# Performance work log

Measured on AMD Instinct MI355X. Metric: run time of the kernel, lower is better.

The kernel has to match this reference:

```python
import jax, jax.numpy as jnp
import numpy as np

LN_EPS = 1e-5
ALPHA_Q = 1.0

def _ln(t, g, b):
    mu = jnp.mean(t, -1, keepdims=True)
    var = jnp.var(t, -1, keepdims=True)
    return (t - mu) / jnp.sqrt(var + LN_EPS) * g + b

def _mlp(t, w1, b1, w2, b2):
    h = jax.nn.gelu(t @ w1.T + b1, approximate=False)
    return h @ w2.T + b2

def setup_inputs() -> dict:
    key = jax.random.key(0)
    B, N, L, E, H, D = 2, 2048, 2048, 1024, 16, 4
    ks = jax.random.split(key, 40)
    rn = lambda i, shape, sc: jax.random.normal(ks[i], shape, jnp.float32) * sc
    inp = {}
    inp['x'] = rn(0, (B, N, E), 1.0)
    inp['xp'] = jax.random.uniform(ks[1], (B, N, D), jnp.float32)
    inp['y'] = rn(2, (B, L, E), 1.0)
    inp['yp'] = jax.random.uniform(ks[3], (B, L, D), jnp.float32)
    inp['attn_mask'] = jax.random.uniform(ks[4], (1, 1, N, L), jnp.float32)
    # PositionEncoder params (torch Linear convention: weight [out,in])
    inp['p_w1'] = rn(5, (E, D), 1.0 / D)
    inp['p_b1'] = jax.random.uniform(ks[6], (E,), jnp.float32, 0.0, np.pi)
    inp['p_w2'] = rn(7, (E, D), 1.0 / D)
    inp['p_b2'] = jax.random.uniform(ks[8], (E,), jnp.float32, 0.0, np.pi)
    # QueryEncoder: LayerNorm + mlp1 + mlp2 (mlp0 is dead code in the source)
    inp['q_ln_g'] = jnp.ones((E,), jnp.float32); inp['q_ln_b'] = jnp.zeros((E,), jnp.float32)
    inp['q_m1_w1'] = rn(9, (2 * E, E), 0.02); inp['q_m1_b1'] = jnp.zeros((2 * E,), jnp.float32)
    inp['q_m1_w2'] = rn(10, (E, 2 * E), 0.02); inp['q_m1_b2'] = jnp.zeros((E,), jnp.float32)
    inp['q_m2_w1'] = rn(11, (2 * E, E), 0.02); inp['q_m2_b1'] = jnp.zeros((2 * E,), jnp.float32)
    inp['q_m2_w2'] = rn(12, (E, 2 * E), 0.02); inp['q_m2_b2'] = jnp.zeros((E,), jnp.float32)
    # KeyEncoder: LayerNorm + mlp1 (mlp0 dead code)
    inp['k_ln_g'] = jnp.ones((E,), jnp.float32); inp['k_ln_b'] = jnp.zeros((E,), jnp.float32)
    inp['k_m1_w1'] = rn(13, (2 * E, E), 0.02); inp['k_m1_b1'] = jnp.zeros((2 * E,), jnp.float32)
    inp['k_m1_w2'] = rn(14, (E, 2 * E), 0.02); inp['k_m1_b2'] = jnp.zeros((E,), jnp.float32)
    # V: LayerNorm + Linear
    inp['v_ln_g'] = jnp.ones((E,), jnp.float32); inp['v_ln_b'] = jnp.zeros((E,), jnp.float32)
    inp['v_w'] = rn(15, (E, E), 0.02); inp['v_b'] = jnp.zeros((E,), jnp.float32)
    # output projections
    inp['proj1_w'] = rn(16, (E, E), 0.02); inp['proj1_b'] = jnp.zeros((E,), jnp.float32)
    inp['proj2_w'] = rn(17, (E, D * H), 0.02); inp['proj2_b'] = jnp.zeros((E,), jnp.float32)
    return inp

def reference(x, xp, y, yp, attn_mask, p_w1, p_b1, p_w2, p_b2,
              q_ln_g, q_ln_b, q_m1_w1, q_m1_b1, q_m1_w2, q_m1_b2,
              q_m2_w1, q_m2_b1, q_m2_w2, q_m2_b2,
              k_ln_g, k_ln_b, k_m1_w1, k_m1_b1, k_m1_w2, k_m1_b2,
              v_ln_g, v_ln_b, v_w, v_b, proj1_w, proj1_b, proj2_w, proj2_b):
    B, N, E = x.shape
    L = y.shape[1]
    D = xp.shape[2]
    H = proj2_w.shape[1] // D
    C = E // H
    # PositionEncoder: query side with bias, key side without bias
    pxt = ALPHA_Q * xp
    xp1 = pxt @ p_w1.T + p_b1            # [B,N,E]
    xp2 = pxt @ p_w2.T + p_b2
    pyt = ALPHA_Q * yp
    yp1 = pyt @ p_w1.T                   # [B,L,E], no bias
    yp2 = pyt @ p_w2.T
    rh = lambda t: t.reshape(t.shape[0], -1, H, C)
    # QueryEncoder
    xn = _ln(x, q_ln_g, q_ln_b)
    x1 = _mlp(xn, q_m1_w1, q_m1_b1, q_m1_w2, q_m1_b2)
    x2 = _mlp(xn, q_m2_w1, q_m2_b1, q_m2_w2, q_m2_b2)
    q = jnp.concatenate([rh(x1 * jnp.cos(xp1)), rh(x1 * jnp.sin(xp1)),
                         rh(x2 * jnp.cos(xp2)), rh(x2 * jnp.sin(xp2))], axis=-1)  # [B,N,H,4C]
    # KeyEncoder (note: second cos/sin block is the raw position code)
    yn = _ln(y, k_ln_g, k_ln_b)
    y1 = _mlp(yn, k_m1_w1, k_m1_b1, k_m1_w2, k_m1_b2)
    k = jnp.concatenate([rh(y1 * jnp.cos(yp1)), rh(y1 * jnp.sin(yp1)),
                         rh(jnp.cos(yp2)), rh(jnp.sin(yp2))], axis=-1)            # [B,L,H,4C]
    scale = (4 * C) ** (-0.5)
    attn = jax.nn.softmax(jnp.einsum('bnhd,blhd->bhnl', q, k) * scale, axis=-1)
    # masked renormalization (mask applied AFTER softmax)
    eps = min(1e-8, 1.0 / L)
    attn = attn * attn_mask
    attn = attn / (jnp.sum(attn, axis=-1, keepdims=True) + eps)
    # values
    v = (_ln(y, v_ln_g, v_ln_b) @ v_w.T + v_b).reshape(B, L, H, C)
    out1 = jnp.einsum('bhnl,blhc->bnhc', attn, v).reshape(B, N, E) @ proj1_w.T + proj1_b
    out2 = jnp.einsum('bhnl,bld->bnhd', attn, yp) - xp[:, :, None, :]             # [B,N,H,D]
    out2 = out2.reshape(B, N, H * D) @ proj2_w.T + proj2_b
    return (out1 + out2, attn, xp)
```

## Files before the change

### kernel.cpp

```cpp
#include <hip/hip_runtime.h>
#include <math.h>
#include <stdint.h>

#define DEV static __device__ __forceinline__

typedef __bf16 bf16x8 __attribute__((ext_vector_type(8)));
typedef __bf16 bf16x4v __attribute__((ext_vector_type(4)));
typedef float f32x4 __attribute__((ext_vector_type(4)));

constexpr int Nn = 2048, Ll = 2048, Ee = 1024, Hh = 16;
constexpr float SCALE = 0.0625f;

constexpr size_t OFF_XN   = 0;
constexpr size_t OFF_YNK  = 8388608;
constexpr size_t OFF_YNV  = 16777216;
constexpr size_t OFF_H12  = 25165824;
constexpr size_t OFF_H3   = 58720256;
constexpr size_t OFF_X1   = 75497472;
constexpr size_t OFF_X2   = 83886080;
constexpr size_t OFF_Y1   = 92274688;
constexpr size_t OFF_QWS  = 100663296;
constexpr size_t OFF_KWS  = 134217728;
constexpr size_t OFF_VWS  = 167772160;
constexpr size_t OFF_DNV  = 176160768;
constexpr size_t OFF_YPT  = 176422912;
constexpr size_t OFF_MSK  = 176685056;
constexpr size_t OFF_AVZ  = 185073664;
constexpr size_t OFF_W1122= 193986560;
constexpr size_t OFF_W12  = 202375168;
constexpr size_t OFF_W22  = 206569472;
constexpr size_t OFF_WK1  = 210763776;
constexpr size_t OFF_WK2  = 214958080;
constexpr size_t OFF_WV   = 219152384;
constexpr size_t OFF_WP   = 221249536;
constexpr size_t OFF_EM   = 223477760;

DEV void gl2l(const void* g, void* l) {
  __builtin_amdgcn_global_load_lds((const __attribute__((address_space(1))) void*)g,
                                   (__attribute__((address_space(3))) void*)l, 16, 0, 0);
}

DEV float gelu_f(float v) {
  float x = v * 0.70710678118654752f;
  float ax = fabsf(x);
  float t = 1.f / fmaf(0.3275911f, ax, 1.f);
  float y = t * fmaf(t, fmaf(t, fmaf(t, fmaf(t, 1.061405429f, -1.453152027f),
                                     1.421413741f), -0.284496736f), 0.254829592f);
  float er = 1.f - y * __expf(-x * x);
  er = (x < 0.f) ? -er : er;
  return 0.5f * v * (1.f + er);
}

__launch_bounds__(256)
__global__ void prep_all(const float* __restrict__ s0, const float* __restrict__ s1,
                         const float* __restrict__ s2, const float* __restrict__ s3,
                         const float* __restrict__ s4, const float* __restrict__ s5,
                         const float* __restrict__ s6,
                         __bf16* __restrict__ d0, __bf16* __restrict__ d1,
                         __bf16* __restrict__ d2, __bf16* __restrict__ d3,
                         __bf16* __restrict__ d4, __bf16* __restrict__ d5,
                         __bf16* __restrict__ d6,
                         const float* __restrict__ pw1, const float* __restrict__ pw2,
                         __bf16* __restrict__ wp,
                         const float* __restrict__ mask, __bf16* __restrict__ mb,
                         const float* __restrict__ yp, __bf16* __restrict__ ypT) {
  int u = blockIdx.x * 256 + threadIdx.x;
  if (u < 3407872) {
    int seg = u >> 19, r = u & 524287;
    const float* s; __bf16* d;
    if      (seg == 0) { s = s0; d = d0; }
    else if (seg == 1) { s = s1; d = d1; }
    else if (seg == 2) { s = s2; d = d2; }
    else if (seg == 3) { s = s3; d = d3; }
    else if (seg == 4) { s = s4; d = d4; }
    else if (seg == 5) { s = s5; d = d5; }
    else               { s = s6; d = d6; }
    float4 v = ((const float4*)s)[r];
    bf16x4v o; o[0]=(__bf16)v.x; o[1]=(__bf16)v.y; o[2]=(__bf16)v.z; o[3]=(__bf16)v.w;
    ((bf16x4v*)d)[r] = o;
  } else if (u < 3686400) {
    int p = u - 3407872;
    int row = p / 272, c4 = p - row * 272;
    float4 v = (c4 < 256) ? ((const float4*)pw1)[row * 256 + c4]
                          : ((const float4*)pw2)[row * 16 + (c4 - 256)];
    bf16x4v o; o[0]=(__bf16)v.x; o[1]=(__bf16)v.y; o[2]=(__bf16)v.z; o[3]=(__bf16)v.w;
    *(bf16x4v*)(wp + (size_t)row * 1088 + (c4 << 2)) = o;
  } else if (u < 4734976) {
    int q = u - 3686400;
    float4 v = ((const float4*)mask)[q];
    bf16x4v o; o[0]=(__bf16)v.x; o[1]=(__bf16)v.y; o[2]=(__bf16)v.z; o[3]=(__bf16)v.w;
    ((bf16x4v*)mb)[q] = o;
  } else {
    int t0 = (u - 4734976) << 2;
    #pragma unroll
    for (int k = 0; k < 4; k++) {
      int i = t0 + k;
      int b = i >> 13, d = (i >> 11) & 3, l = i & 2047;
      ypT[i] = (__bf16)yp[(((size_t)b << 11) + l) * 4 + d];
    }
  }
}

__launch_bounds__(256)
__global__ void ln_all(const float* __restrict__ x, const float* __restrict__ y,
                       const float* __restrict__ qg, const float* __restrict__ qb,
                       const float* __restrict__ kg, const float* __restrict__ kb,
                       const float* __restrict__ vg, const float* __restrict__ vb,
                       __bf16* __restrict__ xn, __bf16* __restrict__ ynk,
                       __bf16* __restrict__ ynv) {
  const int t = blockIdx.x, tid = threadIdx.x;
  const bool isx = t < 4096;
  const int row = isx ? t : t - 4096;
  const float* src = (isx ? x : y) + (size_t)row * Ee;
  const float4 v = ((const float4*)src)[tid];
  float s = v.x + v.y + v.z + v.w;
  float q = v.x*v.x + v.y*v.y + v.z*v.z + v.w*v.w;
  #pragma unroll
  for (int o = 32; o > 0; o >>= 1) { s += __shfl_down(s, o); q += __shfl_down(q, o); }
  __shared__ float ls[4], lq[4];
  if ((tid & 63) == 0) { ls[tid >> 6] = s; lq[tid >> 6] = q; }
  __syncthreads();
  s = ls[0] + ls[1] + ls[2] + ls[3];
  q = lq[0] + lq[1] + lq[2] + lq[3];
  const float mu = s * (1.f / Ee);
  const float rstd = rsqrtf(q * (1.f / Ee) - mu * mu + 1e-5f);
  const int e0 = tid << 2;
  float h0 = (v.x - mu) * rstd, h1 = (v.y - mu) * rstd,
        h2 = (v.z - mu) * rstd, h3 = (v.w - mu) * rstd;
  if (isx) {
    bf16x4v o;
    o[0] = (__bf16)(h0 * qg[e0]   + qb[e0]);
    o[1] = (__bf16)(h1 * qg[e0+1] + qb[e0+1]);
    o[2] = (__bf16)(h2 * qg[e0+2] + qb[e0+2]);
    o[3] = (__bf16)(h3 * qg[e0+3] + qb[e0+3]);
    *(bf16x4v*)(xn + (size_t)row * Ee + e0) = o;
  } else {
    bf16x4v ok, ov;
    ok[0] = (__bf16)(h0 * kg[e0]   + kb[e0]);
    ok[1] = (__bf16)(h1 * kg[e0+1] + kb[e0+1]);
    ok[2] = (__bf16)(h2 * kg[e0+2] + kb[e0+2]);
    ok[3] = (__bf16)(h3 * kg[e0+3] + kb[e0+3]);
    ov[0] = (__bf16)(h0 * vg[e0]   + vb[e0]);
    ov[1] = (__bf16)(h1 * vg[e0+1] + vb[e0+1]);
    ov[2] = (__bf16)(h2 * vg[e0+2] + vb[e0+2]);
    ov[3] = (__bf16)(h3 * vg[e0+3] + vb[e0+3]);
    *(bf16x4v*)(ynk + (size_t)row * Ee + e0) = ok;
    *(bf16x4v*)(ynv + (size_t)row * Ee + e0) = ov;
  }
}

#define GEMM_CORE_BK64(BM_, A_, lda_, W_, ldw_, K_)                                   \
  const int w = tid >> 6, lane = tid & 63, g = lane >> 4, li = lane & 15;             \
  const int wm = (w >> 2) * (BM_ / 2), wn = (w & 3) << 6;                             \
  constexpr int MI = BM_ / 32;                                                        \
  f32x4 acc[MI][4];                                                                   \
  _Pragma("unroll")                                                                   \
  for (int i = 0; i < MI; i++)                                                        \
    _Pragma("unroll")                                                                 \
    for (int j = 0; j < 4; j++) acc[i][j] = (f32x4)0.f;                               \
  auto stage = [&](int buf, int kt) {                                                 \
    const int col0 = kt << 6;                                                         \
    _Pragma("unroll")                                                                 \
    for (int jj = 0; jj < BM_ / 64; jj++) {                                           \
      int c = (jj << 9) + tid;                                                        \
      int row = c >> 3, sl = c & 7;                                                   \
      int col = col0 + ((sl ^ (row & 7)) << 3);                                       \
      gl2l(A_ + (size_t)(m0 + row) * lda_ + col, (buf ? As1 : As0) + ((c - lane) << 3)); \
    }                                                                                 \
    _Pragma("unroll")                                                                 \
    for (int jj = 0; jj < 4; jj++) {                                                  \
      int c = (jj << 9) + tid;                                                        \
      int row = c >> 3, sl = c & 7;                                                   \
      int col = col0 + ((sl ^ (row & 7)) << 3);                                       \
      gl2l(W_ + (size_t)(n0 + row) * ldw_ + col, (buf ? Bs1 : Bs0) + ((c - lane) << 3)); \
    }                                                                                 \
  };                                                                                  \
  const int NT = (K_) >> 6;                                                           \
  stage(0, 0);                                                                        \
  for (int kt = 0; kt < NT; kt++) {                                                   \
    const int cur = kt & 1;                                                           \
    if (kt + 1 < NT) {                                                                \
      stage(cur ^ 1, kt + 1);                                                         \
      asm volatile("s_waitcnt vmcnt(%0)" :: "i"(BM_ / 64 + 4) : "memory");            \
    } else {                                                                          \
      asm volatile("s_waitcnt vmcnt(0)" ::: "memory");                                \
    }                                                                                 \
    __builtin_amdgcn_s_barrier();                                                     \
    __builtin_amdgcn_sched_barrier(0);                                                \
    const __bf16* Acur = cur ? As1 : As0;                                             \
    const __bf16* Bcur = cur ? Bs1 : Bs0;                                             \
    _Pragma("unroll")                                                                 \
    for (int ks = 0; ks < 2; ks++) {                                                  \
      bf16x8 af[MI], bw[4];                                                           \
      _Pragma("unroll")                                                               \
      for (int i = 0; i < MI; i++) {                                                  \
        int ra = wm + (i << 4) + li;                                                  \
        af[i] = *(const bf16x8*)(Acur + ra * 64 + ((((ks << 2) | g) ^ (ra & 7)) << 3)); \
      }                                                                               \
      _Pragma("unroll")                                                               \
      for (int j = 0; j < 4; j++) {                                                   \
        int rb = wn + (j << 4) + li;                                                  \
        bw[j] = *(const bf16x8*)(Bcur + rb * 64 + ((((ks << 2) | g) ^ (rb & 7)) << 3)); \
      }                                                                               \
      _Pragma("unroll")                                                               \
      for (int i = 0; i < MI; i++)                                                    \
        _Pragma("unroll")                                                             \
        for (int j = 0; j < 4; j++)                                                   \
          acc[i][j] = __builtin_amdgcn_mfma_f32_16x16x32_bf16(af[i], bw[j], acc[i][j], 0, 0, 0); \
    }                                                                                 \
    asm volatile("s_waitcnt lgkmcnt(0)" ::: "memory");                                \
    __builtin_amdgcn_sched_barrier(0);                                                \
    __builtin_amdgcn_s_barrier();                                                     \
  }

__launch_bounds__(512, 2)
__global__ void gemm_mlp1(const __bf16* __restrict__ xn, const __bf16* __restrict__ ynk,
                          const __bf16* __restrict__ w1122, const __bf16* __restrict__ wk1,
                          const float* __restrict__ qb1, const float* __restrict__ qb2,
                          const float* __restrict__ kb1,
                          __bf16* __restrict__ h12, __bf16* __restrict__ h3) {
  __shared__ __align__(16) __bf16 As0[256 * 64];
  __shared__ __align__(16) __bf16 As1[256 * 64];
  __shared__ __align__(16) __bf16 Bs0[256 * 64];
  __shared__ __align__(16) __bf16 Bs1[256 * 64];
  const int tid = threadIdx.x, bid = blockIdx.x;
  if (bid < 256) {
    const int m0 = (bid >> 4) << 8, n0 = (bid & 15) << 8;
    GEMM_CORE_BK64(256, xn, 1024, w1122, 1024, 1024)
    #pragma unroll
    for (int j = 0; j < 4; j++) {
      int n = n0 + wn + (j << 4) + li;
      float bias = (n < 2048) ? qb1[n] : qb2[n - 2048];
      #pragma unroll
      for (int i = 0; i < MI; i++) {
        #pragma unroll
        for (int r = 0; r < 4; r++) {
          int m = m0 + wm + (i << 4) + (g << 2) + r;
          h12[(size_t)m * 4096 + n] = (__bf16)gelu_f(acc[i][j][r] + bias);
        }
      }
    }
  } else {
    const int rr = bid - 256;
    const int m0 = (rr >> 3) << 7, n0 = (rr & 7) << 8;
    GEMM_CORE_BK64(128, ynk, 1024, wk1, 1024, 1024)
    #pragma unroll
    for (int j = 0; j < 4; j++) {
      int n = n0 + wn + (j << 4) + li;
      float bias = kb1[n];
      #pragma unroll
      for (int i = 0; i < MI; i++) {
        #pragma unroll
        for (int r = 0; r < 4; r++) {
          int m = m0 + wm + (i << 4) + (g << 2) + r;
          h3[(size_t)m * 2048 + n] = (__bf16)gelu_f(acc[i][j][r] + bias);
        }
      }
    }
  }
}

__launch_bounds__(512, 2)
__global__ void gemm_mlp2(const __bf16* __restrict__ h12, const __bf16* __restrict__ h3,
                          const __bf16* __restrict__ ynv,
                          const __bf16* __restrict__ w12, const __bf16* __restrict__ w22,
                          const __bf16* __restrict__ wk2, const __bf16* __restrict__ wv,
                          const float* __restrict__ bx1, const float* __restrict__ bx2,
                          const float* __restrict__ by1, const float* __restrict__ bv,
                          __bf16* __restrict__ x1, __bf16* __restrict__ x2,
                          __bf16* __restrict__ y1, __bf16* __restrict__ vT) {
  __shared__ __align__(16) __bf16 As0[256 * 64];
  __shared__ __align__(16) __bf16 As1[256 * 64];
  __shared__ __align__(16) __bf16 Bs0[256 * 64];
  __shared__ __align__(16) __bf16 Bs1[256 * 64];
  const int tid = threadIdx.x, bid = blockIdx.x;
  const int seg = bid >> 6, rr = bid & 63;
  const int m0 = (rr >> 2) << 8, n0 = (rr & 3) << 8;
  const __bf16* A; const __bf16* W; const float* bias; __bf16* out; int lda, K;
  if      (seg == 0) { A = h12;        lda = 4096; W = w12; bias = bx1; out = x1; K = 2048; }
  else if (seg == 1) { A = h12 + 2048; lda = 4096; W = w22; bias = bx2; out = x2; K = 2048; }
  else if (seg == 2) { A = h3;         lda = 2048; W = wk2; bias = by1; out = y1; K = 2048; }
  else               { A = ynv;        lda = 1024; W = wv;  bias = bv;  out = vT; K = 1024; }
  GEMM_CORE_BK64(256, A, lda, W, K, K)
  #pragma unroll
  for (int j = 0; j < 4; j++) {
    int n = n0 + wn + (j << 4) + li;
    float bs = bias[n];
    #pragma unroll
    for (int i = 0; i < MI; i++) {
      #pragma unroll
      for (int r = 0; r < 4; r++) {
        int m = m0 + wm + (i << 4) + (g << 2) + r;
        float v = acc[i][j][r] + bs;
        if (seg == 3) {
          int bb = m >> 11, l = m & 2047, hh = n >> 6, cc = n & 63;
          vT[(((size_t)(bb * Hh + hh) * 64 + cc) << 11) + l] = (__bf16)v;
        } else {
          out[(size_t)m * 1024 + n] = (__bf16)v;
        }
      }
    }
  }
}

__launch_bounds__(256)
__global__ void build_qk(const __bf16* __restrict__ x1, const __bf16* __restrict__ x2,
                         const float* __restrict__ xp,
                         const __bf16* __restrict__ y1, const float* __restrict__ yp,
                         const float* __restrict__ pw1, const float* __restrict__ pb1,
                         const float* __restrict__ pw2, const float* __restrict__ pb2,
                         __bf16* __restrict__ q_ws, __bf16* __restrict__ k_ws) {
  const bool isq = blockIdx.x < 2048;
  const int bid = isq ? blockIdx.x : blockIdx.x - 2048;
  const int t = (bid << 1) + (threadIdx.x >> 7);
  const int tl = threadIdx.x & 127;
  const int b = t >> 11, n = t & 2047;
  const int hh = tl >> 3, ch = tl & 7;
  const int e0 = (hh << 6) + (ch << 3);
  const float* pos = isq ? xp : yp;
  const float p0 = pos[(size_t)t*4], p1 = pos[(size_t)t*4+1],
              p2 = pos[(size_t)t*4+2], p3 = pos[(size_t)t*4+3];
  bf16x8 o0, o1, o2, o3;
  if (isq) {
    bf16x8 v1 = *(const bf16x8*)(x1 + (size_t)t * Ee + e0);
    bf16x8 v2 = *(const bf16x8*)(x2 + (size_t)t * Ee + e0);
    #pragma unroll
    for (int sub = 0; sub < 8; sub++) {
      int e = e0 + sub;
      float a1 = pw1[e*4]*p0 + pw1[e*4+1]*p1 + pw1[e*4+2]*p2 + pw1[e*4+3]*p3 + pb1[e];
      float a2 = pw2[e*4]*p0 + pw2[e*4+1]*p1 + pw2[e*4+2]*p2 + pw2[e*4+3]*p3 + pb2[e];
      float s1, c1, s2, c2;
      __sincosf(a1, &s1, &c1); __sincosf(a2, &s2, &c2);
      float xv1 = (float)v1[sub], xv2 = (float)v2[sub];
      o0[sub] = (__bf16)(xv1 * c1); o1[sub] = (__bf16)(xv1 * s1);
      o2[sub] = (__bf16)(xv2 * c2); o3[sub] = (__bf16)(xv2 * s2);
    }
  } else {
    bf16x8 v1 = *(const bf16x8*)(y1 + (size_t)t * Ee + e0);
    #pragma unroll
    for (int sub = 0; sub < 8; sub++) {
      int e = e0 + sub;
      float a1 = pw1[e*4]*p0 + pw1[e*4+1]*p1 + pw1[e*4+2]*p2 + pw1[e*4+3]*p3;
      float a2 = pw2[e*4]*p0 + pw2[e*4+1]*p1 + pw2[e*4+2]*p2 + pw2[e*4+3]*p3;
      float s1, c1, s2, c2;
      __sincosf(a1, &s1, &c1); __sincosf(a2, &s2, &c2);
      float yv = (float)v1[sub];
      o0[sub] = (__bf16)(yv * c1); o1[sub] = (__bf16)(yv * s1);
      o2[sub] = (__bf16)c2;        o3[sub] = (__bf16)s2;
    }
  }
  const int k = n & 7, bc = ch ^ k;
  __bf16* base = (isq ? q_ws : k_ws) + ((((size_t)b * Hh + hh) * Nn + n) << 8);
  *(bf16x8*)(base + ((bc          ) << 3)) = o0;
  *(bf16x8*)(base + (((8  ^ k) ^ ch) << 3)) = o1;
  *(bf16x8*)(base + (((16 ^ k) ^ ch) << 3)) = o2;
  *(bf16x8*)(base + (((24 ^ k) ^ ch) << 3)) = o3;
}

__launch_bounds__(512, 1)
__global__ void attn_fused(const __bf16* __restrict__ q_ws, const __bf16* __restrict__ k_ws,
                           const __bf16* __restrict__ vT_ws, const __bf16* __restrict__ ypT_g,
                           const __bf16* __restrict__ mask_bf, const float* __restrict__ xp,
                           __bf16* __restrict__ em_g, float* __restrict__ dinv_g,
                           __bf16* __restrict__ avz) {
  __shared__ __align__(16) __bf16 kq[2][32 * 256];
  __shared__ __align__(16) __bf16 ms[2][256 * 32];
  __shared__ __align__(16) __bf16 vt[2][64 * 40];
  __shared__ __align__(16) __bf16 pT[256 * 40];
  __shared__ __align__(16) __bf16 ypl[2][16 * 40];
  const int tid = threadIdx.x, w = tid >> 6, lane = tid & 63, g = lane >> 4, li = lane & 15;
  const int logical = ((blockIdx.x & 7) << 5) + (blockIdx.x >> 3);
  const int bh = logical >> 3, nt = logical & 7;
  const int b = bh >> 4, h = bh & 15;
  const int n0 = nt << 8;
  const __bf16* qb = q_ws + (((size_t)bh * Nn + n0) << 8);
  const __bf16* kb = k_ws + (((size_t)bh * Ll) << 8);
  const __bf16* vb = vT_ws + ((size_t)bh << 17);
  const __bf16* yb = ypT_g + ((size_t)b << 13);
  const __bf16* mb = mask_bf + ((size_t)n0 << 11);

  bf16x8 aq[2][8];
  #pragma unroll
  for (int rf = 0; rf < 2; rf++) {
    const int nloc = (w << 5) + (rf << 4) + li;
    #pragma unroll
    for (int s = 0; s < 8; s++)
      aq[rf][s] = *(const bf16x8*)(qb + ((size_t)nloc << 8) + ((((s << 2) + g) ^ (nloc & 7)) << 3));
  }
  for (int i = tid; i < 960; i += 512) {
    int buf = i / 480, idx = i - buf * 480;
    ypl[buf][160 + idx] = (__bf16)0.f;
  }
  {
    const int vc = tid >> 3, vl = (tid & 7) << 2;
    bf16x4v vreg = *(const bf16x4v*)(vb + ((size_t)vc << 11) + vl);
    bf16x4v ypreg;
    if (tid < 32) ypreg = *(const bf16x4v*)(yb + ((size_t)(tid >> 3) << 11) + ((tid & 7) << 2));
    #pragma unroll
    for (int j = 0; j < 2; j++) {
      int c = (j << 9) + tid;
      gl2l(kb + (size_t)(c >> 5) * 256 + ((c & 31) << 3), kq[0] + ((c - lane) << 3));
      gl2l(mb + (size_t)(c >> 2) * 2048 + ((c & 3) << 3), ms[0] + ((c - lane) << 3));
    }
    *(bf16x4v*)(vt[0] + vc * 40 + vl) = vreg;
    if (tid < 32) *(bf16x4v*)(ypl[0] + (tid >> 3) * 40 + ((tid & 7) << 2)) = ypreg;
  }
  __syncthreads();

  float se[2][4], te[2][4];
  f32x4 accv[2][4], accp[2];
  #pragma unroll
  for (int rf = 0; rf < 2; rf++) {
    #pragma unroll
    for (int r = 0; r < 4; r++) { se[rf][r] = 0.f; te[rf][r] = 0.f; }
    #pragma unroll
    for (int cb = 0; cb < 4; cb++) accv[rf][cb] = (f32x4)0.f;
    accp[rf] = (f32x4)0.f;
  }

  for (int t = 0; t < 64; ++t) {
    const int l0 = t << 5, cur = t & 1, nxt = cur ^ 1;
    const bool more = (t < 63);
    bf16x4v vreg, ypreg;
    if (more) {
      const int l1 = l0 + 32;
      vreg = *(const bf16x4v*)(vb + ((size_t)(tid >> 3) << 11) + l1 + ((tid & 7) << 2));
      if (tid < 32) ypreg = *(const bf16x4v*)(yb + ((size_t)(tid >> 3) << 11) + l1 + ((tid & 7) << 2));
      #pragma unroll
      for (int j = 0; j < 2; j++) {
        int c = (j << 9) + tid;
        gl2l(kb + (size_t)(l1 + (c >> 5)) * 256 + ((c & 31) << 3), kq[nxt] + ((c - lane) << 3));
        gl2l(mb + (size_t)(c >> 2) * 2048 + l1 + ((c & 3) << 3), ms[nxt] + ((c - lane) << 3));
      }
    }
    f32x4 Cs[2][2];
    Cs[0][0] = (f32x4)0.f; Cs[0][1] = (f32x4)0.f; Cs[1][0] = (f32x4)0.f; Cs[1][1] = (f32x4)0.f;
    #pragma unroll
    for (int lb = 0; lb < 2; lb++) {
      const int kr = (lb << 4) + li;
      #pragma unroll
      for (int s = 0; s < 8; s++) {
        bf16x8 bk = *(const bf16x8*)(kq[cur] + kr * 256 + ((((s << 2) + g) ^ (kr & 7)) << 3));
        Cs[0][lb] = __builtin_amdgcn_mfma_f32_16x16x32_bf16(aq[0][s], bk, Cs[0][lb], 0, 0, 0);
        Cs[1][lb] = __builtin_amdgcn_mfma_f32_16x16x32_bf16(aq[1][s], bk, Cs[1][lb], 0, 0, 0);
      }
    }
    #pragma unroll
    for (int rf = 0; rf < 2; rf++) {
      #pragma unroll
      for (int lb = 0; lb < 2; lb++) {
        #pragma unroll
        for (int r = 0; r < 4; r++) {
          const int row = (w << 5) + (rf << 4) + (g << 2) + r;
          float e = __expf(Cs[rf][lb][r] * SCALE);
          float mkv = (float)ms[cur][row * 32 + (lb << 4) + li];
          float em = e * mkv;
          se[rf][r] += e; te[rf][r] += em;
          pT[row * 40 + (lb << 4) + li] = (__bf16)em;
        }
      }
    }
    asm volatile("s_waitcnt lgkmcnt(0)" ::: "memory");
    __builtin_amdgcn_sched_barrier(0);
    #pragma unroll
    for (int j = 0; j < 2; j++) {
      int q = (j << 6) + lane;
      int row = q >> 2, ch = q & 3;
      bf16x8 pv = *(const bf16x8*)(pT + ((w << 5) + row) * 40 + (ch << 3));
      *(bf16x8*)(em_g + ((size_t)bh << 22) + ((size_t)(n0 + (w << 5) + row) << 11) + l0 + (ch << 3)) = pv;
    }
    bf16x8 vv[4];
    #pragma unroll
    for (int cb = 0; cb < 4; cb++)
      vv[cb] = *(const bf16x8*)(vt[cur] + ((cb << 4) + li) * 40 + (g << 3));
    bf16x8 yy = *(const bf16x8*)(ypl[cur] + li * 40 + (g << 3));
    #pragma unroll
    for (int rf = 0; rf < 2; rf++) {
      bf16x8 pa = *(const bf16x8*)(pT + ((w << 5) + (rf << 4) + li) * 40 + (g << 3));
      #pragma unroll
      for (int cb = 0; cb < 4; cb++)
        accv[rf][cb] = __builtin_amdgcn_mfma_f32_16x16x32_bf16(pa, vv[cb], accv[rf][cb], 0, 0, 0);
      accp[rf] = __builtin_amdgcn_mfma_f32_16x16x32_bf16(pa, yy, accp[rf], 0, 0, 0);
    }
    if (more) {
      *(bf16x4v*)(vt[nxt] + (tid >> 3) * 40 + ((tid & 7) << 2)) = vreg;
      if (tid < 32) *(bf16x4v*)(ypl[nxt] + (tid >> 3) * 40 + ((tid & 7) << 2)) = ypreg;
    }
    __syncthreads();
  }

  #pragma unroll
  for (int rf = 0; rf < 2; rf++) {
    #pragma unroll
    for (int r = 0; r < 4; r++) {
      float s = se[rf][r], tt = te[rf][r];
      #pragma unroll
      for (int o = 1; o < 16; o <<= 1) { s += __shfl_xor(s, o); tt += __shfl_xor(tt, o); }
      float dinv = 1.f / (tt + 1e-8f * s);
      const int n = n0 + (w << 5) + (rf << 4) + (g << 2) + r;
      if (li == 0) dinv_g[((size_t)bh << 11) + n] = dinv;
      #pragma unroll
      for (int cb = 0; cb < 4; cb++)
        avz[((size_t)b * Nn + n) * 1088 + (h << 6) + (cb << 4) + li] = (__bf16)(accv[rf][cb][r] * dinv);
      if (li < 4) {
        float z = accp[rf][r] * dinv - xp[(((size_t)b * Nn + n) << 2) + li];
        avz[((size_t)b * Nn + n) * 1088 + 1024 + (h << 2) + li] = (__bf16)z;
      }
    }
  }
}

__launch_bounds__(256)
__global__ void fin_proj(const __bf16* __restrict__ A, const __bf16* __restrict__ W,
                         const float* __restrict__ bias1, const float* __restrict__ bias2,
                         float* __restrict__ out,
                         const __bf16* __restrict__ em_g, const float* __restrict__ dinv_g,
                         float* __restrict__ attn_out,
                         const float* __restrict__ xp, float* __restrict__ xp_out) {
  constexpr int N = 1024, K = 1088;
  __shared__ __align__(16) __bf16 As[2][128 * 32];
  __shared__ __align__(16) __bf16 Bs[2][64 * 32];
  const int tid = threadIdx.x;
  if (blockIdx.x >= 512) {
    const int sbid = blockIdx.x - 512;
    if (sbid < 64) {
      int idx = sbid * 256 + tid;
      ((float4*)xp_out)[idx] = ((const float4*)xp)[idx];
    }
    for (size_t i8 = sbid * 256ul + tid; i8 < 16777216ul; i8 += 524288ul) {
      bf16x8 v = ((const bf16x8*)em_g)[i8];
      float dv = dinv_g[i8 >> 8];
      float4 o0, o1;
      o0.x = (float)v[0] * dv; o0.y = (float)v[1] * dv; o0.z = (float)v[2] * dv; o0.w = (float)v[3] * dv;
      o1.x = (float)v[4] * dv; o1.y = (float)v[5] * dv; o1.z = (float)v[6] * dv; o1.w = (float)v[7] * dv;
      ((float4*)attn_out)[i8 * 2]     = o0;
      ((float4*)attn_out)[i8 * 2 + 1] = o1;
    }
    return;
  }
  const int w = tid >> 6, lane = tid & 63, g = lane >> 4, li = lane & 15;
  const int bt = blockIdx.x >> 4;
  const int m0 = bt << 7, n0 = (blockIdx.x & 15) << 6;
  const int wm = (w >> 1) << 6, wn = (w & 1) << 5;
  f32x4 acc[4][2];
  #pragma unroll
  for (int i = 0; i < 4; i++) { acc[i][0] = (f32x4)0.f; acc[i][1] = (f32x4)0.f; }
  auto stage = [&](int buf, int kt) {
    const int col0 = kt << 5;
    #pragma unroll
    for (int j = 0; j < 2; j++) {
      int c = (j << 8) + tid;
      int row = c >> 2, sl = c & 3;
      int col = col0 + ((sl ^ (row & 3)) << 3);
      gl2l(A + (size_t)(m0 + row) * K + col, As[buf] + ((c - lane) << 3));
    }
    {
      int c = tid;
      int row = c >> 2, sl = c & 3;
      int col = col0 + ((sl ^ (row & 3)) << 3);
      gl2l(W + (size_t)(n0 + row) * K + col, Bs[buf] + ((c - lane) << 3));
    }
  };
  const int NT = K >> 5;
  stage(0, 0);
  for (int kt = 0; kt < NT; kt++) {
    const int cur = kt & 1;
    if (kt + 1 < NT) {
      stage(cur ^ 1, kt + 1);
      asm volatile("s_waitcnt vmcnt(3)" ::: "memory");
    } else {
      asm volatile("s_waitcnt vmcnt(0)" ::: "memory");
    }
    __builtin_amdgcn_s_barrier();
    __builtin_amdgcn_sched_barrier(0);
    bf16x8 af[4], bw[2];
    #pragma unroll
    for (int i = 0; i < 4; i++) {
      int ra = wm + (i << 4) + li;
      af[i] = *(const bf16x8*)(As[cur] + ra * 32 + ((g ^ (ra & 3)) << 3));
    }
    #pragma unroll
    for (int j = 0; j < 2; j++) {
      int rb = wn + (j << 4) + li;
      bw[j] = *(const bf16x8*)(Bs[cur] + rb * 32 + ((g ^ (rb & 3)) << 3));
    }
    #pragma unroll
    for (int i = 0; i < 4; i++)
      #pragma unroll
      for (int j = 0; j < 2; j++)
        acc[i][j] = __builtin_amdgcn_mfma_f32_16x16x32_bf16(af[i], bw[j], acc[i][j], 0, 0, 0);
    asm volatile("s_waitcnt lgkmcnt(0)" ::: "memory");
    __builtin_amdgcn_sched_barrier(0);
    __builtin_amdgcn_s_barrier();
  }
  #pragma unroll
  for (int j = 0; j < 2; j++) {
    int n = n0 + wn + (j << 4) + li;
    float bias = bias1[n] + bias2[n];
    #pragma unroll
    for (int i = 0; i < 4; i++) {
      #pragma unroll
      for (int r = 0; r < 4; r++) {
        int m = m0 + wm + (i << 4) + (g << 2) + r;
        out[(size_t)m * N + n] = acc[i][j][r] + bias;
      }
    }
  }
}

extern "C" void kernel_launch(void* const* d_in, const int* in_sizes, int n_in,
                              void* d_out, int out_size, void* d_ws, size_t ws_size,
                              hipStream_t stream) {
  (void)in_sizes; (void)n_in; (void)out_size; (void)ws_size;
  const float* x       = (const float*)d_in[0];
  const float* xp      = (const float*)d_in[1];
  const float* y       = (const float*)d_in[2];
  const float* yp      = (const float*)d_in[3];
  const float* mask    = (const float*)d_in[4];
  const float* p_w1    = (const float*)d_in[5];
  const float* p_b1    = (const float*)d_in[6];
  const float* p_w2    = (const float*)d_in[7];
  const float* p_b2    = (const float*)d_in[8];
  const float* q_ln_g  = (const float*)d_in[9];
  const float* q_ln_b  = (const float*)d_in[10];
  const float* q_m1_w1 = (const float*)d_in[11];
  const float* q_m1_b1 = (const float*)d_in[12];
  const float* q_m1_w2 = (const float*)d_in[13];
  const float* q_m1_b2 = (const float*)d_in[14];
  const float* q_m2_w1 = (const float*)d_in[15];
  const float* q_m2_b1 = (const float*)d_in[16];
  const float* q_m2_w2 = (const float*)d_in[17];
  const float* q_m2_b2 = (const float*)d_in[18];
  const float* k_ln_g  = (const float*)d_in[19];
  const float* k_ln_b  = (const float*)d_in[20];
  const float* k_m1_w1 = (const float*)d_in[21];
  const float* k_m1_b1 = (const float*)d_in[22];
  const float* k_m1_w2 = (const float*)d_in[23];
  const float* k_m1_b2 = (const float*)d_in[24];
  const float* v_ln_g  = (const float*)d_in[25];
  const float* v_ln_b  = (const float*)d_in[26];
  const float* v_w     = (const float*)d_in[27];
  const float* v_b     = (const float*)d_in[28];
  const float* proj1_w = (const float*)d_in[29];
  const float* proj1_b = (const float*)d_in[30];
  const float* proj2_w = (const float*)d_in[31];
  const float* proj2_b = (const float*)d_in[32];

  char* ws = (char*)d_ws;
  __bf16* xn    = (__bf16*)(ws + OFF_XN);
  __bf16* ynk   = (__bf16*)(ws + OFF_YNK);
  __bf16* ynv   = (__bf16*)(ws + OFF_YNV);
  __bf16* h12   = (__bf16*)(ws + OFF_H12);
  __bf16* h3    = (__bf16*)(ws + OFF_H3);
  __bf16* x1    = (__bf16*)(ws + OFF_X1);
  __bf16* x2    = (__bf16*)(ws + OFF_X2);
  __bf16* y1    = (__bf16*)(ws + OFF_Y1);
  __bf16* q_ws  = (__bf16*)(ws + OFF_QWS);
  __bf16* k_ws  = (__bf16*)(ws + OFF_KWS);
  __bf16* vT_ws = (__bf16*)(ws + OFF_VWS);
  float*  dinv  = (float*)(ws + OFF_DNV);
  __bf16* ypT   = (__bf16*)(ws + OFF_YPT);
  __bf16* mskb  = (__bf16*)(ws + OFF_MSK);
  __bf16* avz   = (__bf16*)(ws + OFF_AVZ);
  __bf16* w1122 = (__bf16*)(ws + OFF_W1122);
  __bf16* w12   = (__bf16*)(ws + OFF_W12);
  __bf16* w22   = (__bf16*)(ws + OFF_W22);
  __bf16* wk1   = (__bf16*)(ws + OFF_WK1);
  __bf16* wk2   = (__bf16*)(ws + OFF_WK2);
  __bf16* wv    = (__bf16*)(ws + OFF_WV);
  __bf16* wp    = (__bf16*)(ws + OFF_WP);
  __bf16* em    = (__bf16*)(ws + OFF_EM);

  float* out0     = (float*)d_out;
  float* attn_out = out0 + (size_t)4194304;
  float* xp_out   = out0 + (size_t)138412032;

  prep_all<<<18512, 256, 0, stream>>>(q_m1_w1, q_m2_w1, q_m1_w2, q_m2_w2, k_m1_w1, k_m1_w2, v_w,
                                      w1122, w1122 + 2097152, w12, w22, wk1, wk2, wv,
                                      proj1_w, proj2_w, wp, mask, mskb, yp, ypT);
  ln_all<<<8192, 256, 0, stream>>>(x, y, q_ln_g, q_ln_b, k_ln_g, k_ln_b, v_ln_g, v_ln_b,
                                   xn, ynk, ynv);
  gemm_mlp1<<<512, 512, 0, stream>>>(xn, ynk, w1122, wk1, q_m1_b1, q_m2_b1, k_m1_b1, h12, h3);
  gemm_mlp2<<<256, 512, 0, stream>>>(h12, h3, ynv, w12, w22, wk2, wv,
                                     q_m1_b2, q_m2_b2, k_m1_b2, v_b, x1, x2, y1, vT_ws);
  build_qk<<<4096, 256, 0, stream>>>(x1, x2, xp, y1, yp, p_w1, p_b1, p_w2, p_b2, q_ws, k_ws);
  attn_fused<<<256, 512, 0, stream>>>(q_ws, k_ws, vT_ws, ypT, mskb, xp, em, dinv, avz);
  fin_proj<<<2560, 256, 0, stream>>>(avz, wp, proj1_b, proj2_b, out0,
                                     em, dinv, attn_out, xp, xp_out);
}
```

Baseline: 697.5 us.

## Restructure MLP GEMM core into four-phase pipelined loop with half-K staging

```diff
diff --git a/kernel.cpp b/kernel.cpp
--- a/kernel.cpp
+++ b/kernel.cpp
@@ -149,68 +149,107 @@
   }
 }
 
-#define GEMM_CORE_BK64(BM_, A_, lda_, W_, ldw_, K_)                                   \
+
+#define STAGE_A(BM_, A_, lda_, kt_, kh_, buf_)                                        \
+  _Pragma("unroll")                                                                   \
+  for (int jj = 0; jj < (BM_) / 128; jj++) {                                          \
+    int c = (jj << 9) + tid;                                                          \
+    int row_ = c >> 2, j_ = c & 3;                                                    \
+    int col_ = ((kt_) << 6) + ((kh_) << 5) + ((j_ ^ (row_ & 3)) << 3);                \
+    gl2l(A_ + (size_t)(m0 + row_) * (lda_) + col_,                                    \
+         As + ((((buf_) << 1) + (kh_)) * ((BM_) * 32)) + (c << 3));                   \
+  }
+
+#define STAGE_B(W_, ldw_, kt_, kh_, buf_)                                             \
+  _Pragma("unroll")                                                                   \
+  for (int jj = 0; jj < 2; jj++) {                                                    \
+    int c = (jj << 9) + tid;                                                          \
+    int row_ = c >> 2, j_ = c & 3;                                                    \
+    int col_ = ((kt_) << 6) + ((kh_) << 5) + ((j_ ^ (row_ & 3)) << 3);                \
+    gl2l(W_ + (size_t)(n0 + row_) * (ldw_) + col_,                                    \
+         Bs + ((((buf_) << 1) + (kh_)) * 8192) + (c << 3));                           \
+  }
+
+#define LOAD_A(BM_, buf_, ks_)                                                        \
+  _Pragma("unroll")                                                                   \
+  for (int i = 0; i < (BM_) / 32; i++) {                                              \
+    int ra = wm + (i << 4) + li;                                                      \
+    af[i] = *(const bf16x8*)(As + ((((buf_) << 1) + (ks_)) * ((BM_) * 32))            \
+             + ra * 32 + ((g ^ (ra & 3)) << 3));                                      \
+  }
+
+#define LOAD_B(buf_, ks_, qn_)                                                        \
+  _Pragma("unroll")                                                                   \
+  for (int jj = 0; jj < 2; jj++) {                                                    \
+    int rb = wn + ((qn_) << 5) + (jj << 4) + li;                                      \
+    bw[jj] = *(const bf16x8*)(Bs + ((((buf_) << 1) + (ks_)) * 8192)                   \
+             + rb * 32 + ((g ^ (rb & 3)) << 3));                                      \
+  }
+
+#define MFMA_Q(BM_, qn_)                                                              \
+  __builtin_amdgcn_s_setprio(1);                                                      \
+  _Pragma("unroll")                                                                   \
+  for (int i = 0; i < (BM_) / 32; i++) {                                              \
+    acc[i][((qn_) << 1)]     = __builtin_amdgcn_mfma_f32_16x16x32_bf16(af[i], bw[0], acc[i][((qn_) << 1)], 0, 0, 0);     \
+    acc[i][((qn_) << 1) + 1] = __builtin_amdgcn_mfma_f32_16x16x32_bf16(af[i], bw[1], acc[i][((qn_) << 1) + 1], 0, 0, 0); \
+  }                                                                                   \
+  __builtin_amdgcn_s_setprio(0);
+
+#define PH_SYNC                                                                       \
+  __builtin_amdgcn_s_barrier();                                                       \
+  asm volatile("s_waitcnt lgkmcnt(0)" ::: "memory");                                  \
+  __builtin_amdgcn_sched_barrier(0);
+
+#define PH_END __builtin_amdgcn_s_barrier();
+
+#define GEMM_PIPE(BM_, A_, lda_, W_, ldw_, K_)                                        \
   const int w = tid >> 6, lane = tid & 63, g = lane >> 4, li = lane & 15;             \
-  const int wm = (w >> 2) * (BM_ / 2), wn = (w & 3) << 6;                             \
-  constexpr int MI = BM_ / 32;                                                        \
-  f32x4 acc[MI][4];                                                                   \
+  const int wm = (w >> 2) * ((BM_) / 2), wn = (w & 3) << 6;                           \
+  constexpr int MI_ = (BM_) / 32;                                                     \
+  constexpr int VMC = (BM_) / 128 + 2;                                                \
+  f32x4 acc[MI_][4];                                                                  \
   _Pragma("unroll")                                                                   \
-  for (int i = 0; i < MI; i++)                                                        \
+  for (int i = 0; i < MI_; i++)                                                       \
     _Pragma("unroll")                                                                 \
     for (int j = 0; j < 4; j++) acc[i][j] = (f32x4)0.f;                               \
-  auto stage = [&](int buf, int kt) {                                                 \
-    const int col0 = kt << 6;                                                         \
-    _Pragma("unroll")                                                                 \
-    for (int jj = 0; jj < BM_ / 64; jj++) {                                           \
-      int c = (jj << 9) + tid;                                                        \
-      int row = c >> 3, sl = c & 7;                                                   \
-      int col = col0 + ((sl ^ (row & 7)) << 3);                                       \
-      gl2l(A_ + (size_t)(m0 + row) * lda_ + col, (buf ? As1 : As0) + ((c - lane) << 3)); \
-    }                                                                                 \
-    _Pragma("unroll")                                                                 \
-    for (int jj = 0; jj < 4; jj++) {                                                  \
-      int c = (jj << 9) + tid;                                                        \
-      int row = c >> 3, sl = c & 7;                                                   \
-      int col = col0 + ((sl ^ (row & 7)) << 3);                                       \
-      gl2l(W_ + (size_t)(n0 + row) * ldw_ + col, (buf ? Bs1 : Bs0) + ((c - lane) << 3)); \
-    }                                                                                 \
-  };                                                                                  \
+                                    \
+  STAGE_A(BM_, A_, lda_, 0, 0, 0) STAGE_B(W_, ldw_, 0, 0, 0)                          \
+  STAGE_A(BM_, A_, lda_, 0, 1, 0) STAGE_B(W_, ldw_, 0, 1, 0)                          \
+  STAGE_A(BM_, A_, lda_, 1, 0, 1) STAGE_B(W_, ldw_, 1, 0, 1)                          \
+  asm volatile("s_waitcnt vmcnt(%0)" :: "i"(VMC) : "memory");                         \
+  __builtin_amdgcn_s_barrier();                                                       \
   const int NT = (K_) >> 6;                                                           \
-  stage(0, 0);                                                                        \
-  for (int kt = 0; kt < NT; kt++) {                                                   \
-    const int cur = kt & 1;                                                           \
-    if (kt + 1 < NT) {                                                                \
-      stage(cur ^ 1, kt + 1);                                                         \
-      asm volatile("s_waitcnt vmcnt(%0)" :: "i"(BM_ / 64 + 4) : "memory");            \
+  bf16x8 af[MI_], bw[2];                                                              \
+  for (int t = 0; t < NT; t++) {                                                      \
+    const int buf = t & 1, nbuf = buf ^ 1;                                            \
+    const bool sB = (t + 1 < NT);                     \
+    const bool sA = (t + 2 < NT);                     \
+                                                            \
+    LOAD_A(BM_, buf, 0) LOAD_B(buf, 0, 0)                                             \
+    if (sB) { STAGE_A(BM_, A_, lda_, t + 1, 1, nbuf) }                                \
+    PH_SYNC MFMA_Q(BM_, 0) PH_END                                                     \
+                                                 \
+    LOAD_B(buf, 0, 1)                                                                 \
+    if (sB) {                                                                         \
+      STAGE_B(W_, ldw_, t + 1, 1, nbuf)                                               \
+      asm volatile("s_waitcnt vmcnt(%0)" :: "i"(VMC) : "memory");                     \
     } else {                                                                          \
       asm volatile("s_waitcnt vmcnt(0)" ::: "memory");                                \
     }                                                                                 \
-    __builtin_amdgcn_s_barrier();                                                     \
-    __builtin_amdgcn_sched_barrier(0);                                                \
-    const __bf16* Acur = cur ? As1 : As0;                                             \
-    const __bf16* Bcur = cur ? Bs1 : Bs0;                                             \
-    _Pragma("unroll")                                                                 \
-    for (int ks = 0; ks < 2; ks++) {                                                  \
-      bf16x8 af[MI], bw[4];                                                           \
-      _Pragma("unroll")                                                               \
-      for (int i = 0; i < MI; i++) {                                                  \
-        int ra = wm + (i << 4) + li;                                                  \
-        af[i] = *(const bf16x8*)(Acur + ra * 64 + ((((ks << 2) | g) ^ (ra & 7)) << 3)); \
-      }                                                                               \
-      _Pragma("unroll")                                                               \
-      for (int j = 0; j < 4; j++) {                                                   \
-        int rb = wn + (j << 4) + li;                                                  \
-        bw[j] = *(const bf16x8*)(Bcur + rb * 64 + ((((ks << 2) | g) ^ (rb & 7)) << 3)); \
-      }                                                                               \
-      _Pragma("unroll")                                                               \
-      for (int i = 0; i < MI; i++)                                                    \
-        _Pragma("unroll")                                                             \
-        for (int j = 0; j < 4; j++)                                                   \
-          acc[i][j] = __builtin_amdgcn_mfma_f32_16x16x32_bf16(af[i], bw[j], acc[i][j], 0, 0, 0); \
+    PH_SYNC MFMA_Q(BM_, 1) PH_END                                                     \
+                \
+    LOAD_A(BM_, buf, 1) LOAD_B(buf, 1, 0)                                             \
+    if (sA) { STAGE_A(BM_, A_, lda_, t + 2, 0, buf) }                                 \
+    PH_SYNC MFMA_Q(BM_, 0) PH_END                                                     \
+                                                            \
+    LOAD_B(buf, 1, 1)                                                                 \
+    if (sA) {                                                                         \
+      STAGE_B(W_, ldw_, t + 2, 0, buf)                                                \
+      asm volatile("s_waitcnt vmcnt(%0)" :: "i"(VMC) : "memory");                     \
+    } else if (t + 1 < NT) {                                                          \
+      asm volatile("s_waitcnt vmcnt(0)" ::: "memory");                                \
     }                                                                                 \
-    asm volatile("s_waitcnt lgkmcnt(0)" ::: "memory");                                \
-    __builtin_amdgcn_sched_barrier(0);                                                \
-    __builtin_amdgcn_s_barrier();                                                     \
+    PH_SYNC MFMA_Q(BM_, 1) PH_END                                                     \
   }
 
 __launch_bounds__(512, 2)
@@ -219,20 +258,18 @@
                           const float* __restrict__ qb1, const float* __restrict__ qb2,
                           const float* __restrict__ kb1,
                           __bf16* __restrict__ h12, __bf16* __restrict__ h3) {
-  __shared__ __align__(16) __bf16 As0[256 * 64];
-  __shared__ __align__(16) __bf16 As1[256 * 64];
-  __shared__ __align__(16) __bf16 Bs0[256 * 64];
-  __shared__ __align__(16) __bf16 Bs1[256 * 64];
+  __shared__ __align__(16) __bf16 As[2 * 2 * 256 * 32];
+  __shared__ __align__(16) __bf16 Bs[2 * 2 * 256 * 32];
   const int tid = threadIdx.x, bid = blockIdx.x;
   if (bid < 256) {
     const int m0 = (bid >> 4) << 8, n0 = (bid & 15) << 8;
-    GEMM_CORE_BK64(256, xn, 1024, w1122, 1024, 1024)
+    GEMM_PIPE(256, xn, 1024, w1122, 1024, 1024)
     #pragma unroll
     for (int j = 0; j < 4; j++) {
       int n = n0 + wn + (j << 4) + li;
       float bias = (n < 2048) ? qb1[n] : qb2[n - 2048];
       #pragma unroll
-      for (int i = 0; i < MI; i++) {
+      for (int i = 0; i < MI_; i++) {
         #pragma unroll
         for (int r = 0; r < 4; r++) {
           int m = m0 + wm + (i << 4) + (g << 2) + r;
@@ -243,13 +280,13 @@
   } else {
     const int rr = bid - 256;
     const int m0 = (rr >> 3) << 7, n0 = (rr & 7) << 8;
-    GEMM_CORE_BK64(128, ynk, 1024, wk1, 1024, 1024)
+    GEMM_PIPE(128, ynk, 1024, wk1, 1024, 1024)
     #pragma unroll
     for (int j = 0; j < 4; j++) {
       int n = n0 + wn + (j << 4) + li;
       float bias = kb1[n];
       #pragma unroll
-      for (int i = 0; i < MI; i++) {
+      for (int i = 0; i < MI_; i++) {
         #pragma unroll
         for (int r = 0; r < 4; r++) {
           int m = m0 + wm + (i << 4) + (g << 2) + r;
@@ -269,10 +306,8 @@
                           const float* __restrict__ by1, const float* __restrict__ bv,
                           __bf16* __restrict__ x1, __bf16* __restrict__ x2,
                           __bf16* __restrict__ y1, __bf16* __restrict__ vT) {
-  __shared__ __align__(16) __bf16 As0[256 * 64];
-  __shared__ __align__(16) __bf16 As1[256 * 64];
-  __shared__ __align__(16) __bf16 Bs0[256 * 64];
-  __shared__ __align__(16) __bf16 Bs1[256 * 64];
+  __shared__ __align__(16) __bf16 As[2 * 2 * 256 * 32];
+  __shared__ __align__(16) __bf16 Bs[2 * 2 * 256 * 32];
   const int tid = threadIdx.x, bid = blockIdx.x;
   const int seg = bid >> 6, rr = bid & 63;
   const int m0 = (rr >> 2) << 8, n0 = (rr & 3) << 8;
@@ -281,13 +316,13 @@
   else if (seg == 1) { A = h12 + 2048; lda = 4096; W = w22; bias = bx2; out = x2; K = 2048; }
   else if (seg == 2) { A = h3;         lda = 2048; W = wk2; bias = by1; out = y1; K = 2048; }
   else               { A = ynv;        lda = 1024; W = wv;  bias = bv;  out = vT; K = 1024; }
-  GEMM_CORE_BK64(256, A, lda, W, K, K)
+  GEMM_PIPE(256, A, lda, W, K, K)
   #pragma unroll
   for (int j = 0; j < 4; j++) {
     int n = n0 + wn + (j << 4) + li;
     float bs = bias[n];
     #pragma unroll
-    for (int i = 0; i < MI; i++) {
+    for (int i = 0; i < MI_; i++) {
       #pragma unroll
       for (int r = 0; r < 4; r++) {
         int m = m0 + wm + (i << 4) + (g << 2) + r;
```

After: 694.5 us. Within noise of the previous version (-0.4%).
